# Optimization experiments

Measured on AMD Instinct MI355X. Metric: run time of the kernel, lower is better.

Reference implementation:

```python
import jax, jax.numpy as jnp
import numpy as np

N_HEAD = 16
SIZE_PER_HEAD = 64
NEG_BIG = 1e12


def _len_mask(lengths, T):
    # Faithful to: mask = 1 - cumsum(one_hot(len, T), 1)
    # -> 1.0 for positions < len, 0.0 for positions >= len (all ones if len == T).
    pos = jnp.arange(T)
    return (pos[None, :] < lengths[:, 0, None]).astype(jnp.float32)  # [B, T]


def setup_inputs() -> dict:
    key = jax.random.key(0)
    ks = jax.random.split(key, 8)
    B, T, D = 2, 2048, 1024
    Q_seq = jax.random.normal(ks[0], (B, T, D), dtype=jnp.float32)
    K_seq = jax.random.normal(ks[1], (B, T, D), dtype=jnp.float32)
    V_seq = jax.random.normal(ks[2], (B, T, D), dtype=jnp.float32)
    Q_len = jax.random.randint(ks[3], (B, 1), 0, T, dtype=jnp.int32)
    V_len = jax.random.randint(ks[4], (B, 1), 0, T, dtype=jnp.int32)
    s = 1.0 / np.sqrt(D)
    WQ = jax.random.normal(ks[5], (D, N_HEAD * SIZE_PER_HEAD), dtype=jnp.float32) * s
    WK = jax.random.normal(ks[6], (D, N_HEAD * SIZE_PER_HEAD), dtype=jnp.float32) * s
    WV = jax.random.normal(ks[7], (D, N_HEAD * SIZE_PER_HEAD), dtype=jnp.float32) * s
    return {"Q_seq": Q_seq, "K_seq": K_seq, "V_seq": V_seq,
            "Q_len": Q_len, "V_len": V_len, "WQ": WQ, "WK": WK, "WV": WV}


def reference(Q_seq, K_seq, V_seq, Q_len, V_len, WQ, WK, WV):
    B, Tq, _ = Q_seq.shape
    Tk = K_seq.shape[1]
    H, dh = N_HEAD, SIZE_PER_HEAD

    q = (Q_seq @ WQ).reshape(B, Tq, H, dh)  # [B,Tq,H,dh]
    k = (K_seq @ WK).reshape(B, Tk, H, dh)
    v = (V_seq @ WV).reshape(B, Tk, H, dh)

    # scaled dot-product scores [B,H,Tq,Tk]
    A = jnp.einsum('bqhd,bkhd->bhqk', q, k) / np.sqrt(dh).astype(np.float32)

    # additive key-length mask over the key axis (original: permute+mask+permute)
    kmask = _len_mask(V_len, Tk)  # [B,Tk]
    A = A - (1.0 - kmask)[:, None, None, :] * NEG_BIG
    A = jax.nn.softmax(A, axis=-1)

    O = jnp.einsum('bhqk,bkhd->bqhd', A, v).reshape(B, Tq, H * dh)

    # multiplicative query-length mask
    qmask = _len_mask(Q_len, Tq)  # [B,Tq]
    return O * qmask[:, :, None]
```

## Files before the change

kernel.cpp:

```cpp
#include <hip/hip_runtime.h>


using short8   = __attribute__((ext_vector_type(8))) short;
using floatx4  = __attribute__((ext_vector_type(4))) float;
using floatx16 = __attribute__((ext_vector_type(16))) float;
using uintx4   = __attribute__((ext_vector_type(4))) unsigned int;
using ushort4v = __attribute__((ext_vector_type(4))) unsigned short;

__device__ __forceinline__ unsigned short f2bf(float f) {
    unsigned int u = __builtin_bit_cast(unsigned int, f);
    u += 0x7fffu + ((u >> 16) & 1u);
    return (unsigned short)(u >> 16);
}

__global__ __launch_bounds__(256) void cvt_kernel(
    const float* __restrict__ Qs, const float* __restrict__ Ks,
    const float* __restrict__ Vs, const int* __restrict__ Qlen,
    const int* __restrict__ Vlen, unsigned short* __restrict__ abf)
{
    int z = blockIdx.y, row = blockIdx.x;
    int b = row >> 11, rib = row & 2047;
    int ql = Qlen[b]; int vl = Vlen[b]; int vle = vl ? vl : 2048;
    int lim = (z == 0) ? ((ql + 127) & ~127) : ((vle + 127) & ~127);
    if (rib >= lim) return;
    const float* src = (z == 0) ? Qs : ((z == 1) ? Ks : Vs);
    int t = threadIdx.x;
    float4 v = *reinterpret_cast<const float4*>(src + (size_t)row * 1024 + t * 4);
    ushort4v o;
    o[0] = f2bf(v.x); o[1] = f2bf(v.y); o[2] = f2bf(v.z); o[3] = f2bf(v.w);
    *reinterpret_cast<ushort4v*>(abf + (size_t)z * 4194304u + (size_t)row * 1024 + t * 4) = o;
}

__global__ __launch_bounds__(256) void wt_kernel(
    const float* __restrict__ W0, const float* __restrict__ W1,
    const float* __restrict__ W2, unsigned short* __restrict__ out)
{
    __shared__ float tile[64][65];
    int z = blockIdx.z;
    const float* W = (z == 0) ? W0 : ((z == 1) ? W1 : W2);
    unsigned short* O = out + (size_t)z * 1048576u;
    int r0 = blockIdx.y * 64, c0 = blockIdx.x * 64;
    int t = threadIdx.x;
#pragma unroll
    for (int i = 0; i < 16; i++) {
        int idx = t + i * 256; int r = idx >> 6, c = idx & 63;
        tile[r][c] = W[(size_t)(r0 + r) * 1024 + c0 + c];
    }
    __syncthreads();
#pragma unroll
    for (int i = 0; i < 16; i++) {
        int idx = t + i * 256; int c = idx >> 6, r = idx & 63;
        O[(size_t)(c0 + c) * 1024 + r0 + r] = f2bf(tile[r][c]);
    }
}

template <bool PRECVT>
__global__ __launch_bounds__(256) void proj_kernel(
    const float* __restrict__ Qs, const float* __restrict__ Ks,
    const float* __restrict__ Vs, const unsigned short* __restrict__ abf,
    const unsigned short* __restrict__ wt,
    const int* __restrict__ Qlen, const int* __restrict__ Vlen,
    unsigned short* __restrict__ q, unsigned short* __restrict__ k,
    unsigned short* __restrict__ vT)
{
    __shared__ alignas(16) unsigned short As[128][72];
    __shared__ alignas(16) unsigned short Bs[128][72];

    int z = blockIdx.z;
    int tid = threadIdx.x;
    int m0 = blockIdx.y * 128, n0 = blockIdx.x * 128;
    int b = m0 >> 11, rib = m0 & 2047;
    int ql = Qlen[b]; int vl = Vlen[b]; int vle = vl ? vl : 2048;
    int lim = (z == 0) ? ((ql + 127) & ~127) : ((vle + 127) & ~127);
    if (rib >= lim) return;

    const float* Af = (z == 0) ? Qs : ((z == 1) ? Ks : Vs);
    const unsigned short* Ab = abf + (size_t)z * 4194304u;
    const unsigned short* Bt = wt + (size_t)z * 1048576u;

    int w = tid >> 6, lane = tid & 63, g = lane >> 4, lr = lane & 15;
    int wr = w >> 1, wc = w & 1;

    floatx4 acc[4][4];
#pragma unroll
    for (int m = 0; m < 4; m++)
#pragma unroll
        for (int n = 0; n < 4; n++) {
#pragma unroll
            for (int r = 0; r < 4; r++) acc[m][n][r] = 0.f;
        }

    int srow = tid >> 1, scol = (tid & 1) * 32;

    short8 pa[4], pb[4];
    float4 fa[8];

    if constexpr (PRECVT) {
#pragma unroll
        for (int i = 0; i < 4; i++)
            pa[i] = *reinterpret_cast<const short8*>(Ab + (size_t)(m0 + srow) * 1024 + scol + i * 8);
    } else {
#pragma unroll
        for (int i = 0; i < 8; i++)
            fa[i] = *reinterpret_cast<const float4*>(Af + (size_t)(m0 + srow) * 1024 + scol + i * 4);
    }
#pragma unroll
    for (int i = 0; i < 4; i++)
        pb[i] = *reinterpret_cast<const short8*>(Bt + (size_t)(n0 + srow) * 1024 + scol + i * 8);

    for (int kb = 0; kb < 1024; kb += 64) {
        __syncthreads();
        if constexpr (PRECVT) {
#pragma unroll
            for (int i = 0; i < 4; i++)
                *reinterpret_cast<short8*>(&As[srow][scol + i * 8]) = pa[i];
        } else {
#pragma unroll
            for (int i = 0; i < 4; i++) {
                short8 h;
                h[0] = (short)f2bf(fa[2*i].x);   h[1] = (short)f2bf(fa[2*i].y);
                h[2] = (short)f2bf(fa[2*i].z);   h[3] = (short)f2bf(fa[2*i].w);
                h[4] = (short)f2bf(fa[2*i+1].x); h[5] = (short)f2bf(fa[2*i+1].y);
                h[6] = (short)f2bf(fa[2*i+1].z); h[7] = (short)f2bf(fa[2*i+1].w);
                *reinterpret_cast<short8*>(&As[srow][scol + i * 8]) = h;
            }
        }
#pragma unroll
        for (int i = 0; i < 4; i++)
            *reinterpret_cast<short8*>(&Bs[srow][scol + i * 8]) = pb[i];
        __syncthreads();

        if (kb + 64 < 1024) {
            if constexpr (PRECVT) {
#pragma unroll
                for (int i = 0; i < 4; i++)
                    pa[i] = *reinterpret_cast<const short8*>(Ab + (size_t)(m0 + srow) * 1024 + kb + 64 + scol + i * 8);
            } else {
#pragma unroll
                for (int i = 0; i < 8; i++)
                    fa[i] = *reinterpret_cast<const float4*>(Af + (size_t)(m0 + srow) * 1024 + kb + 64 + scol + i * 4);
            }
#pragma unroll
            for (int i = 0; i < 4; i++)
                pb[i] = *reinterpret_cast<const short8*>(Bt + (size_t)(n0 + srow) * 1024 + kb + 64 + scol + i * 8);
        }

#pragma unroll
        for (int kc = 0; kc < 2; kc++) {
            short8 af[4], bf[4];
#pragma unroll
            for (int m = 0; m < 4; m++)
                af[m] = *reinterpret_cast<const short8*>(&As[wr * 64 + m * 16 + lr][kc * 32 + g * 8]);
#pragma unroll
            for (int n = 0; n < 4; n++)
                bf[n] = *reinterpret_cast<const short8*>(&Bs[wc * 64 + n * 16 + lr][kc * 32 + g * 8]);
#pragma unroll
            for (int m = 0; m < 4; m++)
#pragma unroll
                for (int n = 0; n < 4; n++)
                    acc[m][n] = __builtin_amdgcn_mfma_f32_16x16x32_bf16(af[m], bf[n], acc[m][n], 0, 0, 0);
        }
    }

    if (z < 2) {
        unsigned short* outp = (z == 0) ? q : k;
#pragma unroll
        for (int m = 0; m < 4; m++) {
            int row0 = m0 + wr * 64 + m * 16 + g * 4;
#pragma unroll
            for (int n = 0; n < 4; n++) {
                int col = n0 + wc * 64 + n * 16 + lr;
#pragma unroll
                for (int r = 0; r < 4; r++)
                    outp[(size_t)(row0 + r) * 1024 + col] = f2bf(acc[m][n][r]);
            }
        }
    } else {
#pragma unroll
        for (int m = 0; m < 4; m++) {
            int row0 = m0 + wr * 64 + m * 16 + g * 4;
            int bb = row0 >> 11, t0 = row0 & 2047;
#pragma unroll
            for (int n = 0; n < 4; n++) {
                int col = n0 + wc * 64 + n * 16 + lr;
                ushort4v pk;
#pragma unroll
                for (int r = 0; r < 4; r++) pk[r] = f2bf(acc[m][n][r]);
                *reinterpret_cast<ushort4v*>(vT + (size_t)(bb * 1024 + col) * 2048 + t0) = pk;
            }
        }
    }
}

__global__ __launch_bounds__(128, 2) void attn_kernel(
    const unsigned short* __restrict__ q, const unsigned short* __restrict__ k,
    const unsigned short* __restrict__ vT, const int* __restrict__ Qlen,
    const int* __restrict__ Vlen, float* __restrict__ out)
{
    __shared__ float obuf[64][33];
    __shared__ float mlm[2][33];
    __shared__ float mll[2][33];

    int tid = threadIdx.x;
    int w = tid >> 6, lane = tid & 63;
    int j = lane & 31, hi = lane >> 5;

    int blk = blockIdx.x;
    int x = blk & 7, idx = blk >> 3;
    int bh = x + 8 * (idx >> 6), qtile = idx & 63;
    int b = bh >> 4, h = bh & 15;
    int qlen = Qlen[b]; int vl = Vlen[b]; int vle = vl ? vl : 2048;
    int qrow0 = qtile * 32;

    if (qrow0 >= qlen) {
        int zr = qrow0 + (tid >> 2);
        float* p = out + (size_t)(b * 2048 + zr) * 1024 + h * 64 + (tid & 3) * 16;
        float4 z4; z4.x = 0.f; z4.y = 0.f; z4.z = 0.f; z4.w = 0.f;
#pragma unroll
        for (int s = 0; s < 4; s++) *reinterpret_cast<float4*>(p + 4 * s) = z4;
        return;
    }

    int nt = (vle + 63) >> 6;
    int ntw = (nt - w + 1) >> 1;

    const unsigned short* kbase = k + (size_t)(b * 2048) * 1024 + h * 64 + hi * 8;
    const unsigned short* vbase = vT + (size_t)(b * 1024 + h * 64 + j) * 2048 + hi * 8;

    short8 kf0[4], kf1[4], vf0[4], vf1[4];
    {
        int t0 = (w < nt) ? w : (nt - 1);
        int kt = t0 << 6;
        const unsigned short* kr0 = kbase + (size_t)(kt + j) * 1024;
        const unsigned short* kr1 = kbase + (size_t)(kt + 32 + j) * 1024;
#pragma unroll
        for (int c = 0; c < 4; c++) {
            kf0[c] = *reinterpret_cast<const short8*>(kr0 + c * 16);
            kf1[c] = *reinterpret_cast<const short8*>(kr1 + c * 16);
            vf0[c] = *reinterpret_cast<const short8*>(vbase + kt + c * 16);
            vf1[c] = *reinterpret_cast<const short8*>(vbase + 32 * 2048 + kt + c * 16);
        }
    }
    __builtin_amdgcn_sched_barrier(0);

    short8 qf[4];
    {
        const unsigned short* qp = q + (size_t)(b * 2048 + qrow0 + j) * 1024 + h * 64 + hi * 8;
#pragma unroll
        for (int c = 0; c < 4; c++) qf[c] = *reinterpret_cast<const short8*>(qp + c * 16);
    }

    floatx16 O0, O1;
#pragma unroll
    for (int t = 0; t < 16; t++) { O0[t] = 0.f; O1[t] = 0.f; }
    float m_r = -3.0e38f, l_r = 0.f;

    const float CEXP = 0.18033688011112042f;

    for (int m = 0; m < ntw; ++m) {
        int tix = w + 2 * m;
        int kt = tix << 6;
        int tnx = tix + 2; if (tnx >= nt) tnx = nt - 1;
        int ktn = tnx << 6;

        floatx16 s0, s1;
#pragma unroll
        for (int t = 0; t < 16; t++) { s0[t] = 0.f; s1[t] = 0.f; }
#pragma unroll
        for (int c = 0; c < 4; c++) {
            s0 = __builtin_amdgcn_mfma_f32_32x32x16_bf16(kf0[c], qf[c], s0, 0, 0, 0);
            s1 = __builtin_amdgcn_mfma_f32_32x32x16_bf16(kf1[c], qf[c], s1, 0, 0, 0);
        }

        {
            const unsigned short* kr0 = kbase + (size_t)(ktn + j) * 1024;
            const unsigned short* kr1 = kbase + (size_t)(ktn + 32 + j) * 1024;
#pragma unroll
            for (int c = 0; c < 4; c++) {
                kf0[c] = *reinterpret_cast<const short8*>(kr0 + c * 16);
                kf1[c] = *reinterpret_cast<const short8*>(kr1 + c * 16);
            }
        }
        __builtin_amdgcn_sched_barrier(0);

        if (kt + 64 > vle) {
#pragma unroll
            for (int t = 0; t < 16; t++) {
                int kl = (t & 3) + 8 * (t >> 2) + 4 * hi;
                if (kt + kl >= vle)      s0[t] = -8.0e12f;
                if (kt + 32 + kl >= vle) s1[t] = -8.0e12f;
            }
        }

        float mx = s0[0];
#pragma unroll
        for (int t = 1; t < 16; t++) mx = fmaxf(mx, s0[t]);
#pragma unroll
        for (int t = 0; t < 16; t++) mx = fmaxf(mx, s1[t]);
        float lm = fmaxf(mx, __shfl_xor(mx, 32));

        if (__any(lm > m_r + 64.f)) {
            float mn = fmaxf(m_r, lm);
            float al = __builtin_amdgcn_exp2f((m_r - mn) * CEXP);
            m_r = mn;
            l_r *= al;
#pragma unroll
            for (int t = 0; t < 16; t++) { O0[t] *= al; O1[t] *= al; }
        }
        float nm = -m_r * CEXP;
#pragma unroll
        for (int t = 0; t < 16; t++) {
            s0[t] = __builtin_amdgcn_exp2f(fmaf(s0[t], CEXP, nm));
            s1[t] = __builtin_amdgcn_exp2f(fmaf(s1[t], CEXP, nm));
        }
        float rs = 0.f;
#pragma unroll
        for (int t = 0; t < 16; t++) rs += s0[t] + s1[t];
        l_r += rs;

        unsigned int pbw[4][4];
        {
            unsigned int D[4][2];
#pragma unroll
            for (int s = 0; s < 4; s++) {
                asm("v_cvt_pk_bf16_f32 %0, %1, %2" : "=v"(D[s][0]) : "v"(s0[4*s+0]), "v"(s0[4*s+1]));
                asm("v_cvt_pk_bf16_f32 %0, %1, %2" : "=v"(D[s][1]) : "v"(s0[4*s+2]), "v"(s0[4*s+3]));
            }
#pragma unroll
            for (int u = 0; u < 2; u++) {
                asm volatile("v_permlane32_swap_b32 %0, %1" : "+v"(D[0][u]), "+v"(D[1][u]));
                asm volatile("v_permlane32_swap_b32 %0, %1" : "+v"(D[2][u]), "+v"(D[3][u]));
                pbw[0][u] = D[0][u]; pbw[0][u + 2] = D[1][u];
                pbw[1][u] = D[2][u]; pbw[1][u + 2] = D[3][u];
            }
#pragma unroll
            for (int s = 0; s < 4; s++) {
                asm("v_cvt_pk_bf16_f32 %0, %1, %2" : "=v"(D[s][0]) : "v"(s1[4*s+0]), "v"(s1[4*s+1]));
                asm("v_cvt_pk_bf16_f32 %0, %1, %2" : "=v"(D[s][1]) : "v"(s1[4*s+2]), "v"(s1[4*s+3]));
            }
#pragma unroll
            for (int u = 0; u < 2; u++) {
                asm volatile("v_permlane32_swap_b32 %0, %1" : "+v"(D[0][u]), "+v"(D[1][u]));
                asm volatile("v_permlane32_swap_b32 %0, %1" : "+v"(D[2][u]), "+v"(D[3][u]));
                pbw[2][u] = D[0][u]; pbw[2][u + 2] = D[1][u];
                pbw[3][u] = D[2][u]; pbw[3][u + 2] = D[3][u];
            }
        }

#pragma unroll
        for (int c = 0; c < 4; c++) {
            uintx4 pw; pw[0] = pbw[c][0]; pw[1] = pbw[c][1]; pw[2] = pbw[c][2]; pw[3] = pbw[c][3];
            short8 pf = __builtin_bit_cast(short8, pw);
            O0 = __builtin_amdgcn_mfma_f32_32x32x16_bf16(vf0[c], pf, O0, 0, 0, 0);
            O1 = __builtin_amdgcn_mfma_f32_32x32x16_bf16(vf1[c], pf, O1, 0, 0, 0);
        }

#pragma unroll
        for (int c = 0; c < 4; c++) {
            vf0[c] = *reinterpret_cast<const short8*>(vbase + ktn + c * 16);
            vf1[c] = *reinterpret_cast<const short8*>(vbase + 32 * 2048 + ktn + c * 16);
        }
        __builtin_amdgcn_sched_barrier(0);
    }

    l_r = l_r + __shfl_xor(l_r, 32);
    if (hi == 0) mlm[w][j] = m_r;
    __syncthreads();
    float M = fmaxf(mlm[0][j], mlm[1][j]);
    float al = __builtin_amdgcn_exp2f((m_r - M) * CEXP);
#pragma unroll
    for (int t = 0; t < 16; t++) { O0[t] *= al; O1[t] *= al; }
    if (hi == 0) mll[w][j] = l_r * al;
    if (w == 1) {
#pragma unroll
        for (int t = 0; t < 16; t++) {
            obuf[lane][t]      = O0[t];
            obuf[lane][t + 16] = O1[t];
        }
    }
    __syncthreads();
    if (w == 0) {
#pragma unroll
        for (int t = 0; t < 16; t++) {
            O0[t] += obuf[lane][t];
            O1[t] += obuf[lane][t + 16];
        }
        float lt = mll[0][j] + mll[1][j];
        int qrow = qrow0 + j;
        float qm = (qrow < qlen) ? (1.0f / lt) : 0.f;
        float* ob = out + (size_t)(b * 2048 + qrow) * 1024 + h * 64;
#pragma unroll
        for (int s = 0; s < 4; s++) {
            float4 oa, obv;
            oa.x = O0[4*s+0] * qm; oa.y = O0[4*s+1] * qm; oa.z = O0[4*s+2] * qm; oa.w = O0[4*s+3] * qm;
            obv.x = O1[4*s+0] * qm; obv.y = O1[4*s+1] * qm; obv.z = O1[4*s+2] * qm; obv.w = O1[4*s+3] * qm;
            *reinterpret_cast<float4*>(ob + 8 * s + 4 * hi) = oa;
            *reinterpret_cast<float4*>(ob + 32 + 8 * s + 4 * hi) = obv;
        }
    }
}

extern "C" void kernel_launch(void* const* d_in, const int* in_sizes, int n_in,
                              void* d_out, int out_size, void* d_ws, size_t ws_size,
                              hipStream_t stream)
{
    const float* Q_seq = (const float*)d_in[0];
    const float* K_seq = (const float*)d_in[1];
    const float* V_seq = (const float*)d_in[2];
    const int*   Q_len = (const int*)d_in[3];
    const int*   V_len = (const int*)d_in[4];
    const float* WQ    = (const float*)d_in[5];
    const float* WK    = (const float*)d_in[6];
    const float* WV    = (const float*)d_in[7];
    float* outp = (float*)d_out;

    unsigned short* wsb = (unsigned short*)d_ws;
    unsigned short* wt  = wsb;
    unsigned short* qp  = wsb + (size_t)3 * 1048576u;
    unsigned short* kp  = qp + 4194304u;
    unsigned short* vTp = kp + 4194304u;
    unsigned short* abf = vTp + 4194304u;

    size_t need = ((size_t)3 * 1048576u + 3u * 4194304u + (size_t)3 * 4194304u) * 2u;
    bool precvt = ws_size >= need;

    wt_kernel<<<dim3(16, 16, 3), 256, 0, stream>>>(WQ, WK, WV, wt);
    if (precvt) {
        cvt_kernel<<<dim3(4096, 3), 256, 0, stream>>>(Q_seq, K_seq, V_seq, Q_len, V_len, abf);
        proj_kernel<true><<<dim3(8, 32, 3), 256, 0, stream>>>(
            Q_seq, K_seq, V_seq, abf, wt, Q_len, V_len, qp, kp, vTp);
    } else {
        proj_kernel<false><<<dim3(8, 32, 3), 256, 0, stream>>>(
            Q_seq, K_seq, V_seq, nullptr, wt, Q_len, V_len, qp, kp, vTp);
    }
    attn_kernel<<<dim3(2048), 128, 0, stream>>>(qp, kp, vTp, Q_len, V_len, outp);
}
```

Baseline: 83.55 us.

## Split attention key loop across eight waves per block with tree reduction

The attention kernel goes from 2 to 8 waves per 32-row query tile. Each wave handles every eighth 64-key tile, and the partial softmax states are merged through a three-stage shared-memory tree reduction. This shortens each block's serial key loop and raises the number of waves in flight. MFMA sections are also wrapped in s_setprio to favour matrix issue. The cost is more reduction work and barriers, a larger LDS footprint, and launch_bounds(512,4) may limit registers per thread and cause spills.

New measurement: 145.6 us. 1.74x slower.

```diff
diff --git a/kernel.cpp b/kernel.cpp
--- a/kernel.cpp
+++ b/kernel.cpp
@@ -192,14 +192,14 @@
     }
 }
 
-__global__ __launch_bounds__(128, 2) void attn_kernel(
+__global__ __launch_bounds__(512, 4) void attn_kernel(
     const unsigned short* __restrict__ q, const unsigned short* __restrict__ k,
     const unsigned short* __restrict__ vT, const int* __restrict__ Qlen,
     const int* __restrict__ Vlen, float* __restrict__ out)
 {
-    __shared__ float obuf[64][33];
-    __shared__ float mlm[2][33];
-    __shared__ float mll[2][33];
+    __shared__ float obuf[4][64][33];
+    __shared__ float mlm[8][33];
+    __shared__ float mll[8][33];
 
     int tid = threadIdx.x;
     int w = tid >> 6, lane = tid & 63;
@@ -213,19 +213,19 @@
     int qrow0 = qtile * 32;
 
     if (qrow0 >= qlen) {
-        int zr = qrow0 + (tid >> 2);
-        float* p = out + (size_t)(b * 2048 + zr) * 1024 + h * 64 + (tid & 3) * 16;
+        int zr = qrow0 + (tid >> 4);
+        float* p = out + (size_t)(b * 2048 + zr) * 1024 + h * 64 + (tid & 15) * 4;
         float4 z4; z4.x = 0.f; z4.y = 0.f; z4.z = 0.f; z4.w = 0.f;
-#pragma unroll
-        for (int s = 0; s < 4; s++) *reinterpret_cast<float4*>(p + 4 * s) = z4;
+        *reinterpret_cast<float4*>(p) = z4;
         return;
     }
 
     int nt = (vle + 63) >> 6;
-    int ntw = (nt - w + 1) >> 1;
+    int ntw = (nt > w) ? ((nt - w + 7) >> 3) : 0;
 
     const unsigned short* kbase = k + (size_t)(b * 2048) * 1024 + h * 64 + hi * 8;
     const unsigned short* vbase = vT + (size_t)(b * 1024 + h * 64 + j) * 2048 + hi * 8;
+    const unsigned short* vbase2 = vbase + 32 * 2048;
 
     short8 kf0[4], kf1[4], vf0[4], vf1[4];
     {
@@ -238,7 +238,7 @@
             kf0[c] = *reinterpret_cast<const short8*>(kr0 + c * 16);
             kf1[c] = *reinterpret_cast<const short8*>(kr1 + c * 16);
             vf0[c] = *reinterpret_cast<const short8*>(vbase + kt + c * 16);
-            vf1[c] = *reinterpret_cast<const short8*>(vbase + 32 * 2048 + kt + c * 16);
+            vf1[c] = *reinterpret_cast<const short8*>(vbase2 + kt + c * 16);
         }
     }
     __builtin_amdgcn_sched_barrier(0);
@@ -258,19 +258,21 @@
     const float CEXP = 0.18033688011112042f;
 
     for (int m = 0; m < ntw; ++m) {
-        int tix = w + 2 * m;
+        int tix = w + 8 * m;
         int kt = tix << 6;
-        int tnx = tix + 2; if (tnx >= nt) tnx = nt - 1;
+        int tnx = tix + 8; if (tnx >= nt) tnx = nt - 1;
         int ktn = tnx << 6;
 
         floatx16 s0, s1;
 #pragma unroll
         for (int t = 0; t < 16; t++) { s0[t] = 0.f; s1[t] = 0.f; }
+        __builtin_amdgcn_s_setprio(1);
 #pragma unroll
         for (int c = 0; c < 4; c++) {
             s0 = __builtin_amdgcn_mfma_f32_32x32x16_bf16(kf0[c], qf[c], s0, 0, 0, 0);
             s1 = __builtin_amdgcn_mfma_f32_32x32x16_bf16(kf1[c], qf[c], s1, 0, 0, 0);
         }
+        __builtin_amdgcn_s_setprio(0);
 
         {
             const unsigned short* kr0 = kbase + (size_t)(ktn + j) * 1024;
@@ -347,6 +349,7 @@
             }
         }
 
+        __builtin_amdgcn_s_setprio(1);
 #pragma unroll
         for (int c = 0; c < 4; c++) {
             uintx4 pw; pw[0] = pbw[c][0]; pw[1] = pbw[c][1]; pw[2] = pbw[c][2]; pw[3] = pbw[c][3];
@@ -354,11 +357,12 @@
             O0 = __builtin_amdgcn_mfma_f32_32x32x16_bf16(vf0[c], pf, O0, 0, 0, 0);
             O1 = __builtin_amdgcn_mfma_f32_32x32x16_bf16(vf1[c], pf, O1, 0, 0, 0);
         }
+        __builtin_amdgcn_s_setprio(0);
 
 #pragma unroll
         for (int c = 0; c < 4; c++) {
             vf0[c] = *reinterpret_cast<const short8*>(vbase + ktn + c * 16);
-            vf1[c] = *reinterpret_cast<const short8*>(vbase + 32 * 2048 + ktn + c * 16);
+            vf1[c] = *reinterpret_cast<const short8*>(vbase2 + ktn + c * 16);
         }
         __builtin_amdgcn_sched_barrier(0);
     }
@@ -366,26 +370,63 @@
     l_r = l_r + __shfl_xor(l_r, 32);
     if (hi == 0) mlm[w][j] = m_r;
     __syncthreads();
-    float M = fmaxf(mlm[0][j], mlm[1][j]);
+    float M = mlm[0][j];
+#pragma unroll
+    for (int ww = 1; ww < 8; ww++) M = fmaxf(M, mlm[ww][j]);
     float al = __builtin_amdgcn_exp2f((m_r - M) * CEXP);
 #pragma unroll
     for (int t = 0; t < 16; t++) { O0[t] *= al; O1[t] *= al; }
     if (hi == 0) mll[w][j] = l_r * al;
+
+    if (w >= 4) {
+#pragma unroll
+        for (int t = 0; t < 16; t++) {
+            obuf[w - 4][lane][t]      = O0[t];
+            obuf[w - 4][lane][t + 16] = O1[t];
+        }
+    }
+    __syncthreads();
+    if (w < 4) {
+#pragma unroll
+        for (int t = 0; t < 16; t++) {
+            O0[t] += obuf[w][lane][t];
+            O1[t] += obuf[w][lane][t + 16];
+        }
+    }
+    __syncthreads();
+    if (w >= 2 && w < 4) {
+#pragma unroll
+        for (int t = 0; t < 16; t++) {
+            obuf[w - 2][lane][t]      = O0[t];
+            obuf[w - 2][lane][t + 16] = O1[t];
+        }
+    }
+    __syncthreads();
+    if (w < 2) {
+#pragma unroll
+        for (int t = 0; t < 16; t++) {
+            O0[t] += obuf[w][lane][t];
+            O1[t] += obuf[w][lane][t + 16];
+        }
+    }
+    __syncthreads();
     if (w == 1) {
 #pragma unroll
         for (int t = 0; t < 16; t++) {
-            obuf[lane][t]      = O0[t];
-            obuf[lane][t + 16] = O1[t];
+            obuf[0][lane][t]      = O0[t];
+            obuf[0][lane][t + 16] = O1[t];
         }
     }
     __syncthreads();
     if (w == 0) {
 #pragma unroll
         for (int t = 0; t < 16; t++) {
-            O0[t] += obuf[lane][t];
-            O1[t] += obuf[lane][t + 16];
-        }
-        float lt = mll[0][j] + mll[1][j];
+            O0[t] += obuf[0][lane][t];
+            O1[t] += obuf[0][lane][t + 16];
+        }
+        float lt = 0.f;
+#pragma unroll
+        for (int ww = 0; ww < 8; ww++) lt += mll[ww][j];
         int qrow = qrow0 + j;
         float qm = (qrow < qlen) ? (1.0f / lt) : 0.f;
         float* ob = out + (size_t)(b * 2048 + qrow) * 1024 + h * 64;
@@ -433,5 +474,5 @@
         proj_kernel<false><<<dim3(8, 32, 3), 256, 0, stream>>>(
             Q_seq, K_seq, V_seq, nullptr, wt, Q_len, V_len, qp, kp, vTp);
     }
-    attn_kernel<<<dim3(2048), 128, 0, stream>>>(qp, kp, vTp, Q_len, V_len, outp);
-}
+    attn_kernel<<<dim3(2048), 512, 0, stream>>>(qp, kp, vTp, Q_len, V_len, outp);
+}
```

## Store Q/K/V projections in head-major layout for contiguous attention loads

Applied to the files above, without the earlier changes.

The projection kernel now writes Q and K as [B,H,T,64] and V as per-head 64x64 transposed tiles instead of row-major [B,T,1024] and a [B,1024,T] transpose. Attention loads of K rows and V tiles then come from contiguous 8KB blocks per head rather than rows strided by 2KB or 4KB, which should improve cache-line and TLB locality in the attention loop. In exchange, the projection epilogue scatters 2-byte stores at a 128-byte stride for Q/K, which may be less coalesced than before.

New measurement: 84.30 us. About the same (+0.9%).

```diff
diff --git a/kernel.cpp b/kernel.cpp
--- a/kernel.cpp
+++ b/kernel.cpp
@@ -61,7 +61,7 @@
     const unsigned short* __restrict__ wt,
     const int* __restrict__ Qlen, const int* __restrict__ Vlen,
     unsigned short* __restrict__ q, unsigned short* __restrict__ k,
-    unsigned short* __restrict__ vT)
+    unsigned short* __restrict__ vh)
 {
     __shared__ alignas(16) unsigned short As[128][72];
     __shared__ alignas(16) unsigned short Bs[128][72];
@@ -167,26 +167,32 @@
 #pragma unroll
         for (int m = 0; m < 4; m++) {
             int row0 = m0 + wr * 64 + m * 16 + g * 4;
+            int tg0 = row0 & 2047;
 #pragma unroll
             for (int n = 0; n < 4; n++) {
                 int col = n0 + wc * 64 + n * 16 + lr;
+                int hh = col >> 6, dd = col & 63;
+                size_t base = ((size_t)(b * 16 + hh) * 2048 + tg0) * 64 + dd;
 #pragma unroll
                 for (int r = 0; r < 4; r++)
-                    outp[(size_t)(row0 + r) * 1024 + col] = f2bf(acc[m][n][r]);
+                    outp[base + (size_t)r * 64] = f2bf(acc[m][n][r]);
             }
         }
     } else {
 #pragma unroll
         for (int m = 0; m < 4; m++) {
             int row0 = m0 + wr * 64 + m * 16 + g * 4;
-            int bb = row0 >> 11, t0 = row0 & 2047;
+            int tg = row0 & 2047;
 #pragma unroll
             for (int n = 0; n < 4; n++) {
                 int col = n0 + wc * 64 + n * 16 + lr;
+                int hh = col >> 6, dd = col & 63;
                 ushort4v pk;
 #pragma unroll
                 for (int r = 0; r < 4; r++) pk[r] = f2bf(acc[m][n][r]);
-                *reinterpret_cast<ushort4v*>(vT + (size_t)(bb * 1024 + col) * 2048 + t0) = pk;
+                size_t addr = ((size_t)(b * 16 + hh) * 32 + (tg >> 6)) * 4096
+                            + (size_t)dd * 64 + (tg & 63);
+                *reinterpret_cast<ushort4v*>(vh + addr) = pk;
             }
         }
     }
@@ -194,7 +200,7 @@
 
 __global__ __launch_bounds__(128, 2) void attn_kernel(
     const unsigned short* __restrict__ q, const unsigned short* __restrict__ k,
-    const unsigned short* __restrict__ vT, const int* __restrict__ Qlen,
+    const unsigned short* __restrict__ vh, const int* __restrict__ Qlen,
     const int* __restrict__ Vlen, float* __restrict__ out)
 {
     __shared__ float obuf[64][33];
@@ -224,28 +230,30 @@
     int nt = (vle + 63) >> 6;
     int ntw = (nt - w + 1) >> 1;
 
-    const unsigned short* kbase = k + (size_t)(b * 2048) * 1024 + h * 64 + hi * 8;
-    const unsigned short* vbase = vT + (size_t)(b * 1024 + h * 64 + j) * 2048 + hi * 8;
+    const unsigned short* khb = k + (size_t)(b * 16 + h) * 131072u + hi * 8;
+    const unsigned short* vhb = vh + (size_t)(b * 16 + h) * 131072u + hi * 8;
 
     short8 kf0[4], kf1[4], vf0[4], vf1[4];
     {
         int t0 = (w < nt) ? w : (nt - 1);
         int kt = t0 << 6;
-        const unsigned short* kr0 = kbase + (size_t)(kt + j) * 1024;
-        const unsigned short* kr1 = kbase + (size_t)(kt + 32 + j) * 1024;
+        const unsigned short* kr0 = khb + (size_t)(kt + j) * 64;
+        const unsigned short* kr1 = khb + (size_t)(kt + 32 + j) * 64;
+        const unsigned short* vt0 = vhb + (size_t)t0 * 4096 + j * 64;
 #pragma unroll
         for (int c = 0; c < 4; c++) {
             kf0[c] = *reinterpret_cast<const short8*>(kr0 + c * 16);
             kf1[c] = *reinterpret_cast<const short8*>(kr1 + c * 16);
-            vf0[c] = *reinterpret_cast<const short8*>(vbase + kt + c * 16);
-            vf1[c] = *reinterpret_cast<const short8*>(vbase + 32 * 2048 + kt + c * 16);
+            vf0[c] = *reinterpret_cast<const short8*>(vt0 + c * 16);
+            vf1[c] = *reinterpret_cast<const short8*>(vt0 + 2048 + c * 16);
         }
     }
     __builtin_amdgcn_sched_barrier(0);
 
     short8 qf[4];
     {
-        const unsigned short* qp = q + (size_t)(b * 2048 + qrow0 + j) * 1024 + h * 64 + hi * 8;
+        const unsigned short* qp = q + (size_t)(b * 16 + h) * 131072u
+                                     + (size_t)(qrow0 + j) * 64 + hi * 8;
 #pragma unroll
         for (int c = 0; c < 4; c++) qf[c] = *reinterpret_cast<const short8*>(qp + c * 16);
     }
@@ -273,8 +281,8 @@
         }
 
         {
-            const unsigned short* kr0 = kbase + (size_t)(ktn + j) * 1024;
-            const unsigned short* kr1 = kbase + (size_t)(ktn + 32 + j) * 1024;
+            const unsigned short* kr0 = khb + (size_t)(ktn + j) * 64;
+            const unsigned short* kr1 = khb + (size_t)(ktn + 32 + j) * 64;
 #pragma unroll
             for (int c = 0; c < 4; c++) {
                 kf0[c] = *reinterpret_cast<const short8*>(kr0 + c * 16);
@@ -355,10 +363,13 @@
             O1 = __builtin_amdgcn_mfma_f32_32x32x16_bf16(vf1[c], pf, O1, 0, 0, 0);
         }
 
-#pragma unroll
-        for (int c = 0; c < 4; c++) {
-            vf0[c] = *reinterpret_cast<const short8*>(vbase + ktn + c * 16);
-            vf1[c] = *reinterpret_cast<const short8*>(vbase + 32 * 2048 + ktn + c * 16);
+        {
+            const unsigned short* vt = vhb + (size_t)tnx * 4096 + j * 64;
+#pragma unroll
+            for (int c = 0; c < 4; c++) {
+                vf0[c] = *reinterpret_cast<const short8*>(vt + c * 16);
+                vf1[c] = *reinterpret_cast<const short8*>(vt + 2048 + c * 16);
+            }
         }
         __builtin_amdgcn_sched_barrier(0);
     }
@@ -418,8 +429,8 @@
     unsigned short* wt  = wsb;
     unsigned short* qp  = wsb + (size_t)3 * 1048576u;
     unsigned short* kp  = qp + 4194304u;
-    unsigned short* vTp = kp + 4194304u;
-    unsigned short* abf = vTp + 4194304u;
+    unsigned short* vhp = kp + 4194304u;
+    unsigned short* abf = vhp + 4194304u;
 
     size_t need = ((size_t)3 * 1048576u + 3u * 4194304u + (size_t)3 * 4194304u) * 2u;
     bool precvt = ws_size >= need;
@@ -428,10 +439,10 @@
     if (precvt) {
         cvt_kernel<<<dim3(4096, 3), 256, 0, stream>>>(Q_seq, K_seq, V_seq, Q_len, V_len, abf);
         proj_kernel<true><<<dim3(8, 32, 3), 256, 0, stream>>>(
-            Q_seq, K_seq, V_seq, abf, wt, Q_len, V_len, qp, kp, vTp);
+            Q_seq, K_seq, V_seq, abf, wt, Q_len, V_len, qp, kp, vhp);
     } else {
         proj_kernel<false><<<dim3(8, 32, 3), 256, 0, stream>>>(
-            Q_seq, K_seq, V_seq, nullptr, wt, Q_len, V_len, qp, kp, vTp);
-    }
-    attn_kernel<<<dim3(2048), 128, 0, stream>>>(qp, kp, vTp, Q_len, V_len, outp);
-}
+            Q_seq, K_seq, V_seq, nullptr, wt, Q_len, V_len, qp, kp, vhp);
+    }
+    attn_kernel<<<dim3(2048), 128, 0, stream>>>(qp, kp, vhp, Q_len, V_len, outp);
+}
```
